# Performance work log

Measured on AMD Instinct MI355X. Metric: run time of the kernel, lower is better.

## Reference

```python
import jax, jax.numpy as jnp
import numpy as np
import math

B, S, D, H = 8, 512, 1024, 16
HD = D // H  # 64
FF = 4 * D
EPS = 1e-5


def setup_inputs() -> dict:
    key = jax.random.key(0)
    ks = jax.random.split(key, 12)
    sc = 0.02
    return {
        "x":   jax.random.normal(ks[0], (B, S, D), jnp.float32),
        "Wq":  jax.random.normal(ks[1], (H, D, HD), jnp.float32) * sc,
        "Wk":  jax.random.normal(ks[2], (H, D, HD), jnp.float32) * sc,
        "Wv":  jax.random.normal(ks[3], (H, D, HD), jnp.float32) * sc,
        "Wo":  jax.random.normal(ks[4], (D, D), jnp.float32) * sc,
        "bo":  jnp.zeros((D,), jnp.float32),
        "g1":  jnp.ones((D,), jnp.float32),
        "b1":  jnp.zeros((D,), jnp.float32),
        "g2":  jnp.ones((D,), jnp.float32),
        "b2":  jnp.zeros((D,), jnp.float32),
        "W1":  jax.random.normal(ks[5], (D, FF), jnp.float32) * sc,
        "bf1": jnp.zeros((FF,), jnp.float32),
        "W2":  jax.random.normal(ks[6], (FF, D), jnp.float32) * sc,
        "bf2": jnp.zeros((D,), jnp.float32),
    }


def _layernorm(x, gamma, beta):
    # biased variance, matches torch.var(correction=0)
    mean = jnp.mean(x, axis=-1, keepdims=True)
    var = jnp.mean((x - mean) ** 2, axis=-1, keepdims=True)
    return (x - mean) / jnp.sqrt(var + EPS) * gamma + beta


def _block(x, Wq, Wk, Wv, Wo, bo, g1, b1, g2, b2, W1, bf1, W2, bf2):
    h = _layernorm(x, g1, b1)
    # per-head projections (no bias): [B,H,S,HD]
    Q = jnp.einsum("bsd,hde->bhse", h, Wq)
    K = jnp.einsum("bsd,hde->bhse", h, Wk)
    V = jnp.einsum("bsd,hde->bhse", h, Wv)
    scores = jnp.einsum("bhse,bhte->bhst", Q, K) / math.sqrt(HD)
    causal = jnp.triu(jnp.ones((S, S), bool), k=1)  # upper-triangular masked
    scores = jnp.where(causal, jnp.float32(-1e10), scores)
    att = jax.nn.softmax(scores, axis=-1)  # dropout in eval mode = identity
    ctx = jnp.einsum("bhst,bhte->bhse", att, V)
    # concat heads in order -> [B,S,D]
    ctx = ctx.transpose(0, 2, 1, 3).reshape(B, S, D)
    attn_out = ctx @ Wo + bo
    cache = attn_out + x
    h2 = _layernorm(cache, g2, b2)
    ff = jax.nn.gelu(h2 @ W1 + bf1, approximate=False) @ W2 + bf2
    return ff + cache


def reference(x, Wq, Wk, Wv, Wo, bo, g1, b1, g2, b2, W1, bf1, W2, bf2):
    return _block(x, Wq, Wk, Wv, Wo, bo, g1, b1, g2, b2, W1, bf1, W2, bf2)
```

## Files before the change

kernel.cpp:

```cpp
#include <hip/hip_runtime.h>
#include <hip/hip_bf16.h>

typedef __hip_bfloat16 bf16;

#define B_   8
#define S_   512
#define D_   1024
#define H_   16
#define HD_  64
#define FF_  4096
#define ROWS (B_ * S_)

typedef __attribute__((ext_vector_type(8))) unsigned short u16x8;
typedef __attribute__((ext_vector_type(4))) float f32x4;

typedef __attribute__((address_space(1))) const unsigned int GU32;
typedef __attribute__((address_space(3))) unsigned int LU32;
__device__ __forceinline__ void gld16(const void* g, void* l) {
    __builtin_amdgcn_global_load_lds((GU32*)g, (LU32*)l, 16, 0, 0);
}

__device__ __forceinline__ float bf2f(unsigned short u) {
    union { unsigned int i; float f; } v; v.i = ((unsigned int)u) << 16; return v.f;
}
__device__ __forceinline__ unsigned short f2bfu(float f) {
    bf16 h = __float2bfloat16(f);
    return *reinterpret_cast<unsigned short*>(&h);
}
__device__ __forceinline__ float ldsel(const void* p, size_t i, bool f32) {
    return f32 ? ((const float*)p)[i]
               : __bfloat162float(((const bf16*)p)[i]);
}
__device__ __forceinline__ float gelu_exact(float x) {
    return 0.5f * x * (1.f + erff(x * 0.70710678118654752440f));
}

__global__ __launch_bounds__(256) void ln_kernel(const void* __restrict__ x,
                                                 const void* __restrict__ gam,
                                                 const void* __restrict__ bet,
                                                 bf16* __restrict__ out,
                                                 int x_ws,
                                                 const unsigned short* __restrict__ probe) {
    bool pf32 = (probe[0] == 0);
    bool xf32 = (!x_ws) && pf32;
    int row = blockIdx.x;
    int tid = threadIdx.x;
    size_t rb = (size_t)row * D_;
    float v[4];
#pragma unroll
    for (int i = 0; i < 4; ++i) v[i] = ldsel(x, rb + tid + i * 256, xf32);
    float s  = v[0] + v[1] + v[2] + v[3];
    float s2 = v[0] * v[0] + v[1] * v[1] + v[2] * v[2] + v[3] * v[3];
#pragma unroll
    for (int off = 32; off > 0; off >>= 1) {
        s  += __shfl_down(s, off);
        s2 += __shfl_down(s2, off);
    }
    __shared__ float red[8];
    int wv = tid >> 6, ln = tid & 63;
    if (ln == 0) { red[wv] = s; red[4 + wv] = s2; }
    __syncthreads();
    s  = red[0] + red[1] + red[2] + red[3];
    s2 = red[4] + red[5] + red[6] + red[7];
    float mean = s * (1.f / 1024.f);
    float var  = s2 * (1.f / 1024.f) - mean * mean;
    float rstd = rsqrtf(var + 1e-5f);
#pragma unroll
    for (int i = 0; i < 4; ++i) {
        int c = tid + i * 256;
        float g = ldsel(gam, c, pf32), b = ldsel(bet, c, pf32);
        out[rb + c] = __float2bfloat16((v[i] - mean) * rstd * g + b);
    }
}

__device__ __forceinline__ void transpose_body(
    const void* src, bf16* dst, int bid, int N, int K, int sK, int sH, bool pf32) {
    int tilesN = N >> 6;
    int tn = bid % tilesN, tk = bid / tilesN;
    int n0 = tn * 64, k0 = tk * 64;
    __shared__ float T[64][65];
    int t = threadIdx.x;
    size_t headoff = (size_t)(n0 >> 6) * sH;
#pragma unroll
    for (int i = 0; i < 16; ++i) {
        int lin = t + i * 256;
        int kl = lin >> 6, nl = lin & 63;
        size_t e = headoff + (size_t)(k0 + kl) * sK + nl;
        T[kl][nl] = ldsel(src, e, pf32);
    }
    __syncthreads();
#pragma unroll
    for (int i = 0; i < 16; ++i) {
        int lin = t + i * 256;
        int nl = lin >> 6, kl = lin & 63;
        dst[(size_t)(n0 + nl) * K + k0 + kl] = __float2bfloat16(T[kl][nl]);
    }
}

__global__ __launch_bounds__(256) void transpose_kernel(
    const void* __restrict__ src, bf16* __restrict__ dst,
    int N, int K, int sK, int sH,
    const unsigned short* __restrict__ probe) {
    transpose_body(src, dst, blockIdx.x, N, K, sK, sH, probe[0] == 0);
}

__global__ __launch_bounds__(256) void transpose3_kernel(
    const void* __restrict__ s0, const void* __restrict__ s1,
    const void* __restrict__ s2, bf16* __restrict__ dst,
    const unsigned short* __restrict__ probe) {
    int which = blockIdx.x >> 8;
    const void* src = (which == 0) ? s0 : ((which == 1) ? s1 : s2);
    transpose_body(src, dst + (size_t)which * 1024 * 1024,
                   blockIdx.x & 255, 1024, 1024, HD_, D_ * HD_, probe[0] == 0);
}

template<int BN>
__global__ __launch_bounds__(256) void gemm_mfma(
    const bf16* __restrict__ A, const bf16* __restrict__ Bt,
    int K, int nSeg, int segShift, size_t segStride,
    const void* __restrict__ bias,
    const void* __restrict__ resid, int resid_ws,
    bf16* __restrict__ outWS, void* __restrict__ outFinal, int mode,
    const unsigned short* __restrict__ probe) {
    constexpr int BM     = 128;
    constexpr int NR     = BN / 32;
    constexpr int PLANES = (BN == 64) ? 2 : 1;
    constexpr int KSTEP  = 32 * PLANES;
    constexpr int CPP    = 8 + BN / 16;
    constexpr int NCH    = PLANES * CPP / 4;
    constexpr int APL    = BM * 32;
    constexpr int BPL    = BN * 32;
    constexpr int AREG   = 2 * PLANES * APL;
    bool pf32 = (probe[0] == 0);
    __shared__ alignas(16) unsigned short SMEM[2 * PLANES * (BM + BN) * 32];
    int tid  = threadIdx.x;
    int lane = tid & 63, wv = tid >> 6;
    int g = lane >> 4, i16 = lane & 15;
    int wrow = wv >> 1, wcol = wv & 1;

    int GX = gridDim.x, GY = gridDim.y;
    int T = GX * GY;
    int bid = blockIdx.y * GX + blockIdx.x;
    int bm, bn;
    if (((T & 7) == 0) && ((GY & 3) == 0) && ((GX & 1) == 0)) {
        int x = bid & 7, rank = bid >> 3;
        int xr = x >> 1, xc = x & 1;
        int MS = GY >> 2, NS = GX >> 1;
        int G = (NS % 8 == 0) ? 8 : ((NS % 6 == 0) ? 6 : NS);
        int ng = rank / (MS * G);
        int rem = rank - ng * (MS * G);
        int mloc = rem / G, nloc = ng * G + (rem - (rem / G) * G);
        bm = xr * MS + mloc; bn = xc * NS + nloc;
    } else { bm = blockIdx.y; bn = blockIdx.x; }
    int m0 = bm * BM, n0 = bn * BN;

    f32x4 acc[4][NR];
#pragma unroll
    for (int i = 0; i < 4; ++i)
#pragma unroll
        for (int j = 0; j < NR; ++j) acc[i][j] = (f32x4){0.f, 0.f, 0.f, 0.f};

    const unsigned short* gsrc[NCH];
    unsigned short* l0[NCH];
    unsigned short* l1[NCH];
    {
        int rl = lane >> 2, kq = (lane & 3) * 8;
#pragma unroll
        for (int c0 = 0; c0 < NCH; ++c0) {
            int c = c0 * 4 + wv;
            int pl = c / CPP, cc = c - pl * CPP;
            if (cc < 8) {
                gsrc[c0] = (const unsigned short*)A
                         + (size_t)(m0 + cc * 16 + rl) * K + pl * 32 + kq;
                l0[c0] = &SMEM[(0 * PLANES + pl) * APL + cc * 512];
                l1[c0] = &SMEM[(1 * PLANES + pl) * APL + cc * 512];
            } else {
                gsrc[c0] = (const unsigned short*)Bt
                         + (size_t)(n0 + (cc - 8) * 16 + rl) * K + pl * 32 + kq;
                l0[c0] = &SMEM[AREG + (0 * PLANES + pl) * BPL + (cc - 8) * 512];
                l1[c0] = &SMEM[AREG + (1 * PLANES + pl) * BPL + (cc - 8) * 512];
            }
        }
    }

#define STAGE0(KOFF) { _Pragma("unroll") \
    for (int c0 = 0; c0 < NCH; ++c0) gld16(gsrc[c0] + (KOFF), l0[c0]); }
#define STAGE1(KOFF) { _Pragma("unroll") \
    for (int c0 = 0; c0 < NCH; ++c0) gld16(gsrc[c0] + (KOFF), l1[c0]); }
#define COMPUTE(BUF) { \
    _Pragma("unroll") \
    for (int pl = 0; pl < PLANES; ++pl) { \
        u16x8 af[4], bfv[NR]; \
        _Pragma("unroll") \
        for (int i = 0; i < 4; ++i) \
            af[i] = *reinterpret_cast<const u16x8*>( \
                &SMEM[((BUF) * PLANES + pl) * APL + (wrow * 64 + i * 16 + i16) * 32 + g * 8]); \
        _Pragma("unroll") \
        for (int j = 0; j < NR; ++j) \
            bfv[j] = *reinterpret_cast<const u16x8*>( \
                &SMEM[AREG + ((BUF) * PLANES + pl) * BPL + (wcol * (BN / 2) + j * 16 + i16) * 32 + g * 8]); \
        _Pragma("unroll") \
        for (int i = 0; i < 4; ++i) \
            _Pragma("unroll") \
            for (int j = 0; j < NR; ++j) \
                asm("v_mfma_f32_16x16x32_bf16 %0, %1, %2, %0" \
                    : "+v"(acc[i][j]) : "v"(af[i]), "v"(bfv[j])); \
    } }

    STAGE0(0);
    __syncthreads();
    for (int k0 = 0; k0 < K; k0 += 2 * KSTEP) {
        STAGE1(k0 + KSTEP);
        COMPUTE(0);
        __syncthreads();
        if (k0 + 2 * KSTEP < K) STAGE0(k0 + 2 * KSTEP);
        COMPUTE(1);
        __syncthreads();
    }
#undef STAGE0
#undef STAGE1
#undef COMPUTE

    __builtin_amdgcn_sched_barrier(0);
    asm volatile("s_nop 7\n\ts_nop 7\n\ts_nop 7" ::: );
    __builtin_amdgcn_sched_barrier(0);

    if (outFinal && pf32) {
        int coll = i16, rowl = g * 4;
#pragma unroll
        for (int j = 0; j < NR; ++j) {
            int n = n0 + wcol * (BN / 2) + j * 16 + coll;
            int nl = n & (nSeg - 1);
            float bval = (mode != 0) ? ldsel(bias, nl, pf32) : 0.f;
#pragma unroll
            for (int i = 0; i < 4; ++i) {
                int mb = m0 + wrow * 64 + i * 16 + rowl;
#pragma unroll
                for (int r = 0; r < 4; ++r) {
                    size_t idx = (size_t)(mb + r) * nSeg + nl;
                    float c = acc[i][j][r];
                    if (mode == 1) {
                        c += bval;
                        c += resid_ws ? __bfloat162float(((const bf16*)resid)[idx])
                                      : ldsel(resid, idx, pf32);
                    } else if (mode == 2) {
                        c = gelu_exact(c + bval);
                    }
                    ((float*)outFinal)[idx] = c;
                }
            }
        }
    } else {
        unsigned short* Cs = SMEM;
        int seg = n0 >> segShift;
        int nl0 = n0 & (nSeg - 1);
        bf16* dst = outFinal ? (bf16*)outFinal
                             : outWS + (size_t)seg * segStride;
#pragma unroll
        for (int j = 0; j < NR; ++j) {
            int nloc = wcol * (BN / 2) + j * 16 + i16;
            int nl = nl0 + nloc;
            float bval = (mode != 0) ? ldsel(bias, nl, pf32) : 0.f;
#pragma unroll
            for (int i = 0; i < 4; ++i) {
#pragma unroll
                for (int r = 0; r < 4; ++r) {
                    int mloc = wrow * 64 + i * 16 + g * 4 + r;
                    float c = acc[i][j][r];
                    if (mode == 1) {
                        size_t idx = (size_t)(m0 + mloc) * nSeg + nl;
                        c += bval;
                        c += resid_ws ? __bfloat162float(((const bf16*)resid)[idx])
                                      : ldsel(resid, idx, pf32);
                    } else if (mode == 2) {
                        c = gelu_exact(c + bval);
                    }
                    int swzC = ((((mloc >> 2) & 3) ^ (mloc & 3)) << 4);
                    Cs[mloc * BN + (nloc ^ swzC)] = f2bfu(c);
                }
            }
        }
        __syncthreads();
        constexpr int NP = (BM * BN) / 2048;
#pragma unroll
        for (int p = 0; p < NP; ++p) {
            int lin = p * 2048 + tid * 8;
            int m = lin / BN, nn = lin % BN;
            int swzC = ((((m >> 2) & 3) ^ (m & 3)) << 4);
            u16x8 v = *reinterpret_cast<const u16x8*>(&Cs[m * BN + (nn ^ swzC)]);
            *reinterpret_cast<u16x8*>(dst + (size_t)(m0 + m) * nSeg + nl0 + nn) = v;
        }
    }
}

__global__ __launch_bounds__(256) void attn_kernel(const bf16* __restrict__ Qg,
                                                   const bf16* __restrict__ Kg,
                                                   const bf16* __restrict__ Vg,
                                                   bf16* __restrict__ Og) {
    constexpr int P = 72;
    __shared__ alignas(16) unsigned short Ks[64 * P];
    __shared__ alignas(16) unsigned short Vt[64 * P];
    __shared__ alignas(16) unsigned short Ps[64 * P];
    int qb = blockIdx.x;
    int bh = blockIdx.y;
    int b = bh >> 4, h = bh & 15;
    int tid = threadIdx.x;
    int lane = tid & 63, wv = tid >> 6;
    int g = lane >> 4, i16 = lane & 15;
    size_t base = ((size_t)b * S_) * D_ + h * HD_;

    u16x8 qa[2];
    {
        const unsigned short* qp = (const unsigned short*)Qg + base
            + (size_t)(qb * 64 + wv * 16 + i16) * D_ + g * 8;
#pragma unroll
        for (int kk = 0; kk < 2; ++kk) {
            u16x8 v = *reinterpret_cast<const u16x8*>(qp + kk * 32);
#pragma unroll
            for (int e = 0; e < 8; ++e) v[e] = f2bfu(bf2f(v[e]) * 0.125f);
            qa[kk] = v;
        }
    }
    f32x4 ov[4];
#pragma unroll
    for (int dj = 0; dj < 4; ++dj) ov[dj] = (f32x4){0.f, 0.f, 0.f, 0.f};
    float mrow[4], lrow[4];
#pragma unroll
    for (int r = 0; r < 4; ++r) { mrow[r] = -1e30f; lrow[r] = 0.f; }

    int st = tid >> 2, sd = (tid & 3) * 16;
    const unsigned short* Kp = (const unsigned short*)Kg + base + (size_t)st * D_ + sd;
    const unsigned short* Vp = (const unsigned short*)Vg + base + (size_t)st * D_ + sd;
    unsigned short* KsW = &Ks[st * P + sd];
    unsigned short* VtW = &Vt[sd * P + (st ^ sd)];
    int g1 = g >> 1, g0 = g & 1;
    unsigned short* PsW = &Ps[(wv * 16 + g * 4) * P + (i16 ^ (g0 << 3))];
    const unsigned short* PsR = &Ps[(wv * 16 + i16) * P + ((g ^ ((i16 >> 2) & 3)) << 3)];

    for (int kb = 0; kb <= qb; ++kb) {
        __syncthreads();
        size_t ko = (size_t)kb * 64 * D_;
        u16x8 k0 = *reinterpret_cast<const u16x8*>(Kp + ko);
        u16x8 k1 = *reinterpret_cast<const u16x8*>(Kp + ko + 8);
        u16x8 v0 = *reinterpret_cast<const u16x8*>(Vp + ko);
        u16x8 v1 = *reinterpret_cast<const u16x8*>(Vp + ko + 8);
        *reinterpret_cast<u16x8*>(KsW)     = k0;
        *reinterpret_cast<u16x8*>(KsW + 8) = k1;
#pragma unroll
        for (int ii = 0; ii < 8; ++ii) VtW[ii * P] = v0[ii];
#pragma unroll
        for (int ii = 0; ii < 8; ++ii) VtW[(ii + 8) * P] = v1[ii];
        __syncthreads();

        f32x4 sc[4];
#pragma unroll
        for (int tj = 0; tj < 4; ++tj) sc[tj] = (f32x4){0.f, 0.f, 0.f, 0.f};
#pragma unroll
        for (int kk = 0; kk < 2; ++kk)
#pragma unroll
            for (int tj = 0; tj < 4; ++tj) {
                u16x8 kf = *reinterpret_cast<const u16x8*>(
                    &Ks[(tj * 16 + i16) * P + kk * 32 + g * 8]);
                asm("v_mfma_f32_16x16x32_bf16 %0, %1, %2, %0"
                    : "+v"(sc[tj]) : "v"(qa[kk]), "v"(kf));
            }
        __builtin_amdgcn_sched_barrier(0);
        asm volatile("s_nop 7\n\ts_nop 7\n\ts_nop 7" ::: );
        __builtin_amdgcn_sched_barrier(0);

        if (kb == qb) {
#pragma unroll
            for (int tj = 0; tj < 4; ++tj)
#pragma unroll
                for (int r = 0; r < 4; ++r)
                    if (tj * 16 + i16 > wv * 16 + g * 4 + r) sc[tj][r] = -1e30f;
        }
        float al[4];
#pragma unroll
        for (int r = 0; r < 4; ++r) {
            float mt = fmaxf(fmaxf(sc[0][r], sc[1][r]), fmaxf(sc[2][r], sc[3][r]));
            mt = fmaxf(mt, __shfl_xor(mt, 1));
            mt = fmaxf(mt, __shfl_xor(mt, 2));
            mt = fmaxf(mt, __shfl_xor(mt, 4));
            mt = fmaxf(mt, __shfl_xor(mt, 8));
            float mnew = fmaxf(mrow[r], mt);
            al[r] = __expf(mrow[r] - mnew);
            mrow[r] = mnew;
        }
        float psum[4] = {0.f, 0.f, 0.f, 0.f};
        unsigned short pw[4][4];
#pragma unroll
        for (int tj = 0; tj < 4; ++tj)
#pragma unroll
            for (int r = 0; r < 4; ++r) {
                float p = __expf(sc[tj][r] - mrow[r]);
                unsigned short pb = f2bfu(p);
                pw[tj][r] = pb;
                psum[r] += bf2f(pb);
            }
#pragma unroll
        for (int r = 0; r < 4; ++r) {
            float ps = psum[r];
            ps += __shfl_xor(ps, 1);
            ps += __shfl_xor(ps, 2);
            ps += __shfl_xor(ps, 4);
            ps += __shfl_xor(ps, 8);
            lrow[r] = lrow[r] * al[r] + ps;
        }
#pragma unroll
        for (int dj = 0; dj < 4; ++dj)
#pragma unroll
            for (int r = 0; r < 4; ++r) ov[dj][r] *= al[r];
#pragma unroll
        for (int r = 0; r < 4; ++r)
#pragma unroll
            for (int tj = 0; tj < 4; ++tj)
                PsW[r * P + ((tj ^ g1) << 4)] = pw[tj][r];
#pragma unroll
        for (int kk = 0; kk < 2; ++kk) {
            u16x8 pf = *reinterpret_cast<const u16x8*>(PsR + kk * 32);
#pragma unroll
            for (int dj = 0; dj < 4; ++dj) {
                int tcol = ((kk << 5) | (g << 3)) ^ (dj << 4);
                u16x8 vf = *reinterpret_cast<const u16x8*>(
                    &Vt[(dj * 16 + i16) * P + tcol]);
                asm("v_mfma_f32_16x16x32_bf16 %0, %1, %2, %0"
                    : "+v"(ov[dj]) : "v"(pf), "v"(vf));
            }
        }
    }
    __builtin_amdgcn_sched_barrier(0);
    asm volatile("s_nop 7\n\ts_nop 7\n\ts_nop 7" ::: );
    __builtin_amdgcn_sched_barrier(0);
    float rl[4];
#pragma unroll
    for (int r = 0; r < 4; ++r) rl[r] = 1.f / lrow[r];
    bf16* op = Og + base + (size_t)(qb * 64 + wv * 16 + g * 4) * D_ + i16;
#pragma unroll
    for (int r = 0; r < 4; ++r)
#pragma unroll
        for (int dj = 0; dj < 4; ++dj)
            op[(size_t)r * D_ + dj * 16] = __float2bfloat16(ov[dj][r] * rl[r]);
}

extern "C" void kernel_launch(void* const* d_in, const int* in_sizes, int n_in,
                              void* d_out, int out_size, void* d_ws, size_t ws_size,
                              hipStream_t stream) {
    const void* x   = d_in[0];
    const void* Wq  = d_in[1];
    const void* Wk  = d_in[2];
    const void* Wv  = d_in[3];
    const void* Wo  = d_in[4];
    const void* bo  = d_in[5];
    const void* g1  = d_in[6];
    const void* b1  = d_in[7];
    const void* g2  = d_in[8];
    const void* b2  = d_in[9];
    const void* W1  = d_in[10];
    const void* bf1 = d_in[11];
    const void* W2  = d_in[12];
    const void* bf2 = d_in[13];
    const unsigned short* probe = (const unsigned short*)g1;

    bf16* ws = (bf16*)d_ws;
    const size_t Mi = (size_t)1024 * 1024;
    bf16* h     = ws;
    bf16* Qb    = ws + 4 * Mi;
    bf16* Kb    = ws + 8 * Mi;
    bf16* Vb    = ws + 12 * Mi;
    bf16* ctx   = ws;
    bf16* cache = ws + 4 * Mi;
    bf16* h2    = ws + 8 * Mi;
    bf16* ff1   = ws + 12 * Mi;
    bf16* WqT   = ws + 16 * Mi;
    bf16* WoT   = ws + 19 * Mi;
    bf16* W1T   = ws;
    bf16* W2T   = ws + 8 * Mi;

    transpose3_kernel<<<768, 256, 0, stream>>>(Wq, Wk, Wv, WqT, probe);
    transpose_kernel<<<256, 256, 0, stream>>>(Wo, WoT, 1024, 1024, 1024, 64, probe);
    ln_kernel<<<ROWS, 256, 0, stream>>>(x, g1, b1, h, 0, probe);
    gemm_mfma<128><<<dim3(3072 / 128, ROWS / 128), 256, 0, stream>>>(
        h, WqT, 1024, 1024, 10, 4 * Mi,
        nullptr, nullptr, 0, Qb, nullptr, 0, probe);
    dim3 gA(S_ / 64, B_ * H_);
    attn_kernel<<<gA, 256, 0, stream>>>(Qb, Kb, Vb, ctx);
    gemm_mfma<64><<<dim3(1024 / 64, ROWS / 128), 256, 0, stream>>>(
        ctx, WoT, 1024, 1024, 30, 0,
        bo, x, 0, cache, nullptr, 1, probe);
    transpose_kernel<<<1024, 256, 0, stream>>>(W1, W1T, 4096, 1024, FF_, 64, probe);
    ln_kernel<<<ROWS, 256, 0, stream>>>(cache, g2, b2, h2, 1, probe);
    gemm_mfma<128><<<dim3(4096 / 128, ROWS / 128), 256, 0, stream>>>(
        h2, W1T, 1024, 4096, 30, 0,
        bf1, nullptr, 0, ff1, nullptr, 2, probe);
    transpose_kernel<<<1024, 256, 0, stream>>>(W2, W2T, 1024, 4096, 1024, 64, probe);
    gemm_mfma<64><<<dim3(1024 / 64, ROWS / 128), 256, 0, stream>>>(
        ff1, W2T, 4096, 1024, 30, 0,
        bf2, cache, 1, nullptr, d_out, 1, probe);
}
```

Measured before the change: 381.1 us.

## Merge transposes and layernorms into combined prep kernels; widen FF1 GEMM tile

```diff
diff --git a/kernel.cpp b/kernel.cpp
--- a/kernel.cpp
+++ b/kernel.cpp
@@ -35,15 +35,9 @@
     return 0.5f * x * (1.f + erff(x * 0.70710678118654752440f));
 }
 
-__global__ __launch_bounds__(256) void ln_kernel(const void* __restrict__ x,
-                                                 const void* __restrict__ gam,
-                                                 const void* __restrict__ bet,
-                                                 bf16* __restrict__ out,
-                                                 int x_ws,
-                                                 const unsigned short* __restrict__ probe) {
-    bool pf32 = (probe[0] == 0);
-    bool xf32 = (!x_ws) && pf32;
-    int row = blockIdx.x;
+__device__ __forceinline__ void ln_body(const void* x, const void* gam,
+                                        const void* bet, bf16* out,
+                                        int row, bool xf32, bool pf32) {
     int tid = threadIdx.x;
     size_t rb = (size_t)row * D_;
     float v[4];
@@ -104,14 +98,36 @@
     transpose_body(src, dst, blockIdx.x, N, K, sK, sH, probe[0] == 0);
 }
 
-__global__ __launch_bounds__(256) void transpose3_kernel(
-    const void* __restrict__ s0, const void* __restrict__ s1,
-    const void* __restrict__ s2, bf16* __restrict__ dst,
+__global__ __launch_bounds__(256) void prep1_kernel(
+    const void* __restrict__ Wq, const void* __restrict__ Wk,
+    const void* __restrict__ Wv, const void* __restrict__ Wo,
+    const void* __restrict__ x, const void* __restrict__ g1,
+    const void* __restrict__ b1,
+    bf16* __restrict__ WqT, bf16* __restrict__ WoT, bf16* __restrict__ h,
     const unsigned short* __restrict__ probe) {
-    int which = blockIdx.x >> 8;
-    const void* src = (which == 0) ? s0 : ((which == 1) ? s1 : s2);
-    transpose_body(src, dst + (size_t)which * 1024 * 1024,
-                   blockIdx.x & 255, 1024, 1024, HD_, D_ * HD_, probe[0] == 0);
+    bool pf32 = (probe[0] == 0);
+    int bid = blockIdx.x;
+    if (bid < 768) {
+        int which = bid >> 8;
+        const void* src = (which == 0) ? Wq : ((which == 1) ? Wk : Wv);
+        transpose_body(src, WqT + (size_t)which * 1024 * 1024, bid & 255,
+                       1024, 1024, HD_, D_ * HD_, pf32);
+    } else if (bid < 1024) {
+        transpose_body(Wo, WoT, bid - 768, 1024, 1024, 1024, 64, pf32);
+    } else {
+        ln_body(x, g1, b1, h, bid - 1024, pf32, pf32);
+    }
+}
+
+__global__ __launch_bounds__(256) void prep2_kernel(
+    const void* __restrict__ W1, const void* __restrict__ cache_,
+    const void* __restrict__ g2, const void* __restrict__ b2,
+    bf16* __restrict__ W1T, bf16* __restrict__ h2,
+    const unsigned short* __restrict__ probe) {
+    bool pf32 = (probe[0] == 0);
+    int bid = blockIdx.x;
+    if (bid < 1024) transpose_body(W1, W1T, bid, 4096, 1024, FF_, 64, pf32);
+    else            ln_body(cache_, g2, b2, h2, bid - 1024, false, pf32);
 }
 
 template<int BN>
@@ -131,8 +147,10 @@
     constexpr int APL    = BM * 32;
     constexpr int BPL    = BN * 32;
     constexpr int AREG   = 2 * PLANES * APL;
+    constexpr int STG    = 2 * PLANES * (BM + BN) * 32;
+    constexpr int SMEMSZ = (BM * BN > STG) ? (BM * BN) : STG;
     bool pf32 = (probe[0] == 0);
-    __shared__ alignas(16) unsigned short SMEM[2 * PLANES * (BM + BN) * 32];
+    __shared__ alignas(16) unsigned short SMEM[SMEMSZ];
     int tid  = threadIdx.x;
     int lane = tid & 63, wv = tid >> 6;
     int g = lane >> 4, i16 = lane & 15;
@@ -477,9 +495,8 @@
     bf16* W1T   = ws;
     bf16* W2T   = ws + 8 * Mi;
 
-    transpose3_kernel<<<768, 256, 0, stream>>>(Wq, Wk, Wv, WqT, probe);
-    transpose_kernel<<<256, 256, 0, stream>>>(Wo, WoT, 1024, 1024, 1024, 64, probe);
-    ln_kernel<<<ROWS, 256, 0, stream>>>(x, g1, b1, h, 0, probe);
+    prep1_kernel<<<5120, 256, 0, stream>>>(Wq, Wk, Wv, Wo, x, g1, b1,
+                                           WqT, WoT, h, probe);
     gemm_mfma<128><<<dim3(3072 / 128, ROWS / 128), 256, 0, stream>>>(
         h, WqT, 1024, 1024, 10, 4 * Mi,
         nullptr, nullptr, 0, Qb, nullptr, 0, probe);
@@ -488,9 +505,8 @@
     gemm_mfma<64><<<dim3(1024 / 64, ROWS / 128), 256, 0, stream>>>(
         ctx, WoT, 1024, 1024, 30, 0,
         bo, x, 0, cache, nullptr, 1, probe);
-    transpose_kernel<<<1024, 256, 0, stream>>>(W1, W1T, 4096, 1024, FF_, 64, probe);
-    ln_kernel<<<ROWS, 256, 0, stream>>>(cache, g2, b2, h2, 1, probe);
-    gemm_mfma<128><<<dim3(4096 / 128, ROWS / 128), 256, 0, stream>>>(
+    prep2_kernel<<<5120, 256, 0, stream>>>(W1, cache, g2, b2, W1T, h2, probe);
+    gemm_mfma<256><<<dim3(4096 / 256, ROWS / 128), 256, 0, stream>>>(
         h2, W1T, 1024, 4096, 30, 0,
         bf1, nullptr, 0, ff1, nullptr, 2, probe);
     transpose_kernel<<<1024, 256, 0, stream>>>(W2, W2T, 1024, 4096, 1024, 64, probe);
```

New measurement: 386.1 us. Within noise of the previous version (+1.3%).
